# Kernel optimization log

Measured on AMD Instinct MI355X. Metric: run time of the kernel, lower is better.

The kernel has to match this reference:

```python
import jax, jax.numpy as jnp
import numpy as np
import math

B, S, D, H = 2, 2048, 1024, 16
HD = D // H

def setup_inputs() -> dict:
    key = jax.random.key(0)
    ks = jax.random.split(key, 12)
    s = 0.02
    inp = {
        'query': jax.random.normal(ks[0], (B, S, D), jnp.float32),
        'key':   jax.random.normal(ks[1], (B, S, D), jnp.float32),
        'value': jax.random.normal(ks[2], (B, S, D), jnp.float32),
        # causal mask: True = masked out
        'mask': jnp.broadcast_to(~jnp.tril(jnp.ones((S, S), bool)), (B, S, S)),
        'Wq': jax.random.normal(ks[3], (D, D), jnp.float32) * s,
        'bq': jnp.zeros((D,), jnp.float32),
        'Wk': jax.random.normal(ks[4], (D, D), jnp.float32) * s,
        'bk': jnp.zeros((D,), jnp.float32),
        'Wv': jax.random.normal(ks[5], (D, D), jnp.float32) * s,
        'bv': jnp.zeros((D,), jnp.float32),
        'Wo': jax.random.normal(ks[6], (D, D), jnp.float32) * s,
        'bo': jnp.zeros((D,), jnp.float32),
    }
    return inp

def reference(query, key, value, mask, Wq, bq, Wk, bk, Wv, bv, Wo, bo):
    def shape(x):  # [B,S,D] -> [B,H,S,HD]
        return x.reshape(B, -1, H, HD).transpose(0, 2, 1, 3)
    Q = shape(query @ Wq.T + bq) / math.sqrt(HD)
    K = shape(key @ Wk.T + bk)
    V = shape(value @ Wv.T + bv)
    scores = jnp.einsum('bhqd,bhkd->bhqk', Q, K).astype(jnp.float32)
    scores = jnp.where(mask[:, None, :, :], -1e18, scores)
    attn = jax.nn.softmax(scores, axis=-1).astype(query.dtype)
    # dropout p=0 (inference)
    ctx = jnp.einsum('bhqk,bhkd->bhqd', attn, V)
    ctx = ctx.transpose(0, 2, 1, 3).reshape(B, -1, D)
    output = ctx @ Wo.T + bo
    return output, attn
```

## Files before the change

kernel.cpp:

```cpp
#include <hip/hip_runtime.h>
#include <hip/hip_fp16.h>

typedef _Float16 f16;
typedef f16 f16x8 __attribute__((ext_vector_type(8)));
typedef float f32x4 __attribute__((ext_vector_type(4)));

#define MFMA16(a, b, c) __builtin_amdgcn_mfma_f32_16x16x32_f16(a, b, c, 0, 0, 0)

static constexpr int Bn = 2, Sn = 2048, Dn = 1024, Hn = 16, HDn = 64;
static constexpr int Mn = Bn * Sn;

__device__ inline void gload_lds16(const void* g, void* l) {
    __builtin_amdgcn_global_load_lds((const __attribute__((address_space(1))) void*)g,
                                     (__attribute__((address_space(3))) void*)l,
                                     16, 0, 0);
}

__global__ __launch_bounds__(256) void convert_all(
    const float* __restrict__ q, const float* __restrict__ k, const float* __restrict__ v,
    const float* __restrict__ wq, const float* __restrict__ wk, const float* __restrict__ wv,
    const float* __restrict__ wo,
    f16* qo, f16* ko, f16* vo, f16* wqo, f16* wko, f16* wvo, f16* woo) {
    const int c = blockIdx.x * 256 + threadIdx.x;
    const float* src;
    f16* dst;
    int off;
    if (c < 3 * 524288) {
        const int t = c >> 19;
        off = c & 524287;
        src = (t == 0) ? q : (t == 1) ? k : v;
        dst = (t == 0) ? qo : (t == 1) ? ko : vo;
    } else {
        const int c2 = c - 3 * 524288;
        const int t = c2 >> 17;
        off = c2 & 131071;
        src = (t == 0) ? wq : (t == 1) ? wk : (t == 2) ? wv : wo;
        dst = (t == 0) ? wqo : (t == 1) ? wko : (t == 2) ? wvo : woo;
    }
    const float4 a = ((const float4*)src)[off * 2];
    const float4 b = ((const float4*)src)[off * 2 + 1];
    f16x8 r = {(f16)a.x, (f16)a.y, (f16)a.z, (f16)a.w,
               (f16)b.x, (f16)b.y, (f16)b.z, (f16)b.w};
    *(f16x8*)(dst + (size_t)off * 8) = r;
}

struct GemmArgs {
    const f16* X[3];
    const f16* W[3];
    const float* bias[3];
    void* out[3];
    float scale[3];
};

template <bool OUT_F16>
__global__ __launch_bounds__(256) void gemm128(GemmArgs args) {
    __shared__ __align__(16) f16 sbuf[2 * 128 * 64];
    f16* As = sbuf;
    f16* Bs = sbuf + 128 * 64;

    const int z = blockIdx.z;
    const f16* __restrict__ X = args.X[z];
    const f16* __restrict__ W = args.W[z];
    const float* __restrict__ bias = args.bias[z];
    const float scale = args.scale[z];

    const int tid = threadIdx.x, w = tid >> 6, lane = tid & 63;
    const int lr = lane & 15, lg = lane >> 4;
    const int m0 = blockIdx.y * 128, n0 = blockIdx.x * 128;
    const int wm = (w >> 1) * 64, wn = (w & 1) * 64;

    const int srow = w * 32 + (lane >> 3);
    const int scol = (lane & 7) * 8;

    f32x4 acc[4][4] = {};

    for (int k0 = 0; k0 < Dn; k0 += 64) {
        __syncthreads();
#pragma unroll
        for (int j = 0; j < 4; ++j) {
            gload_lds16(X + (size_t)(m0 + srow + j * 8) * Dn + k0 + scol,
                        &As[(w * 4 + j) * 512]);
            gload_lds16(W + (size_t)(n0 + srow + j * 8) * Dn + k0 + scol,
                        &Bs[(w * 4 + j) * 512]);
        }
        __syncthreads();

#pragma unroll
        for (int half = 0; half < 2; ++half) {
            f16x8 a[4], b[4];
#pragma unroll
            for (int mi = 0; mi < 4; ++mi)
                a[mi] = *(const f16x8*)&As[(wm + mi * 16 + lr) * 64 + half * 32 + lg * 8];
#pragma unroll
            for (int ni = 0; ni < 4; ++ni)
                b[ni] = *(const f16x8*)&Bs[(wn + ni * 16 + lr) * 64 + half * 32 + lg * 8];
#pragma unroll
            for (int mi = 0; mi < 4; ++mi)
#pragma unroll
                for (int ni = 0; ni < 4; ++ni)
                    acc[mi][ni] = MFMA16(a[mi], b[ni], acc[mi][ni]);
        }
    }

    float bv[4];
#pragma unroll
    for (int ni = 0; ni < 4; ++ni) bv[ni] = bias[n0 + wn + ni * 16 + lr];

    if (OUT_F16) {
        __syncthreads();
#pragma unroll
        for (int mi = 0; mi < 4; ++mi)
#pragma unroll
            for (int ni = 0; ni < 4; ++ni)
#pragma unroll
                for (int j = 0; j < 4; ++j)
                    sbuf[(wm + mi * 16 + lg * 4 + j) * 128 + wn + ni * 16 + lr] =
                        (f16)((acc[mi][ni][j] + bv[ni]) * scale);
        __syncthreads();
        f16* out = (f16*)args.out[z];
#pragma unroll
        for (int t = 0; t < 8; ++t) {
            const int idx = t * 256 + tid;
            const int r = idx >> 4, cc = (idx & 15) * 8;
            *(f16x8*)(out + (size_t)(m0 + r) * Dn + n0 + cc) = *(f16x8*)&sbuf[r * 128 + cc];
        }
    } else {
        float* out = (float*)args.out[z];
#pragma unroll
        for (int mi = 0; mi < 4; ++mi)
#pragma unroll
            for (int ni = 0; ni < 4; ++ni)
#pragma unroll
                for (int j = 0; j < 4; ++j)
                    out[(size_t)(m0 + wm + mi * 16 + lg * 4 + j) * Dn + n0 + wn + ni * 16 + lr] =
                        (acc[mi][ni][j] + bv[ni]) * scale;
    }
}

__global__ __launch_bounds__(256) void flash_ctx(const f16* __restrict__ Qh,
                                                 const f16* __restrict__ Kh,
                                                 const f16* __restrict__ Vh,
                                                 f16* __restrict__ ctx,
                                                 float* __restrict__ rinv_g) {
    __shared__ __align__(16) f16 Qs[64][72];
    __shared__ __align__(16) f16 Ks[64][72];
    __shared__ __align__(16) f16 Vs[64][72];
    __shared__ __align__(16) f16 Ps[4][16][72];

    const int tid = threadIdx.x, w = tid >> 6, lane = tid & 63;
    const int lr = lane & 15, lg = lane >> 4;
    const int qt = blockIdx.x;
    const int bh = blockIdx.y;
    const int b = bh >> 4, h = bh & 15;

    const f16* Qb = Qh + (size_t)b * Sn * Dn + h * HDn;
    const f16* Kb = Kh + (size_t)b * Sn * Dn + h * HDn;
    const f16* Vb = Vh + (size_t)b * Sn * Dn + h * HDn;

    for (int i = tid; i < 512; i += 256) {
        const int r = i >> 3, dq = i & 7;
        *(f16x8*)&Qs[r][dq * 8] = *(const f16x8*)(Qb + (size_t)(qt * 64 + r) * Dn + dq * 8);
    }
    __syncthreads();
    f16x8 qa0 = *(const f16x8*)&Qs[w * 16 + lr][lg * 8];
    f16x8 qa1 = *(const f16x8*)&Qs[w * 16 + lr][lg * 8 + 32];

    float lsum[4] = {0.f, 0.f, 0.f, 0.f};
    f32x4 octx[4] = {};

    for (int kt = 0; kt <= qt; ++kt) {
        __syncthreads();
        for (int i = tid; i < 512; i += 256) {
            const int r = i >> 3, dq = i & 7;
            *(f16x8*)&Ks[r][dq * 8] = *(const f16x8*)(Kb + (size_t)(kt * 64 + r) * Dn + dq * 8);
        }
        for (int i = tid; i < 512; i += 256) {
            const int kk = i & 63, dq = i >> 6;
            f16x8 v = *(const f16x8*)(Vb + (size_t)(kt * 64 + kk) * Dn + dq * 8);
#pragma unroll
            for (int j = 0; j < 8; ++j) Vs[dq * 8 + j][kk] = v[j];
        }
        __syncthreads();

        const bool diag = (kt == qt);
#pragma unroll
        for (int nf = 0; nf < 4; ++nf) {
            f16x8 kb0 = *(const f16x8*)&Ks[nf * 16 + lr][lg * 8];
            f16x8 kb1 = *(const f16x8*)&Ks[nf * 16 + lr][lg * 8 + 32];
            f32x4 a = {};
            a = MFMA16(qa0, kb0, a);
            a = MFMA16(qa1, kb1, a);
#pragma unroll
            for (int j = 0; j < 4; ++j) {
                const int qr = w * 16 + lg * 4 + j;
                const int kc = nf * 16 + lr;
                const bool masked = diag && (kc > qr);
                const float p = masked ? 0.f : __expf(a[j]);
                lsum[j] += p;
                Ps[w][lg * 4 + j][kc] = (f16)p;
            }
        }

        f16x8 pa0 = *(const f16x8*)&Ps[w][lr][lg * 8];
        f16x8 pa1 = *(const f16x8*)&Ps[w][lr][lg * 8 + 32];
#pragma unroll
        for (int df = 0; df < 4; ++df) {
            f16x8 vb0 = *(const f16x8*)&Vs[df * 16 + lr][lg * 8];
            f16x8 vb1 = *(const f16x8*)&Vs[df * 16 + lr][lg * 8 + 32];
            octx[df] = MFMA16(pa0, vb0, octx[df]);
            octx[df] = MFMA16(pa1, vb1, octx[df]);
        }
    }

    float rv[4];
#pragma unroll
    for (int j = 0; j < 4; ++j) {
        float s = lsum[j];
        s += __shfl_xor(s, 1);
        s += __shfl_xor(s, 2);
        s += __shfl_xor(s, 4);
        s += __shfl_xor(s, 8);
        rv[j] = 1.0f / s;
    }

#pragma unroll
    for (int df = 0; df < 4; ++df) {
#pragma unroll
        for (int j = 0; j < 4; ++j) {
            const int sq = qt * 64 + w * 16 + lg * 4 + j;
            const int d = df * 16 + lr;
            ctx[((size_t)b * Sn + sq) * Dn + h * HDn + d] = (f16)(octx[df][j] * rv[j]);
        }
    }
    if (lr == 0) {
#pragma unroll
        for (int j = 0; j < 4; ++j)
            rinv_g[(size_t)bh * Sn + qt * 64 + w * 16 + lg * 4 + j] = rv[j];
    }
}

__global__ __launch_bounds__(256) void attn_write(const f16* __restrict__ Qh,
                                                  const f16* __restrict__ Kh,
                                                  const float* __restrict__ rinv_g,
                                                  float* __restrict__ attn) {
    __shared__ __align__(16) f16 Qs[64][72];
    __shared__ __align__(16) f16 Ks[64][72];
    __shared__ __align__(16) float Pf[64][68];

    const int tid = threadIdx.x, w = tid >> 6, lane = tid & 63;
    const int lr = lane & 15, lg = lane >> 4;
    const int qt = blockIdx.x;
    const int bh = blockIdx.y;
    const int b = bh >> 4, h = bh & 15;

    const f16* Qb = Qh + (size_t)b * Sn * Dn + h * HDn;
    const f16* Kb = Kh + (size_t)b * Sn * Dn + h * HDn;
    float* attn_base = attn + ((size_t)bh * Sn + qt * 64) * Sn;

    for (int i = tid; i < 512; i += 256) {
        const int r = i >> 3, dq = i & 7;
        *(f16x8*)&Qs[r][dq * 8] = *(const f16x8*)(Qb + (size_t)(qt * 64 + r) * Dn + dq * 8);
    }

    float rv[4];
#pragma unroll
    for (int j = 0; j < 4; ++j)
        rv[j] = rinv_g[(size_t)bh * Sn + qt * 64 + w * 16 + lg * 4 + j];

    __syncthreads();
    f16x8 qa0 = *(const f16x8*)&Qs[w * 16 + lr][lg * 8];
    f16x8 qa1 = *(const f16x8*)&Qs[w * 16 + lr][lg * 8 + 32];

    for (int kt = 0; kt <= qt; ++kt) {
        __syncthreads();
        for (int i = tid; i < 512; i += 256) {
            const int r = i >> 3, dq = i & 7;
            *(f16x8*)&Ks[r][dq * 8] = *(const f16x8*)(Kb + (size_t)(kt * 64 + r) * Dn + dq * 8);
        }
        __syncthreads();

        const bool diag = (kt == qt);
#pragma unroll
        for (int nf = 0; nf < 4; ++nf) {
            f16x8 kb0 = *(const f16x8*)&Ks[nf * 16 + lr][lg * 8];
            f16x8 kb1 = *(const f16x8*)&Ks[nf * 16 + lr][lg * 8 + 32];
            f32x4 a = {};
            a = MFMA16(qa0, kb0, a);
            a = MFMA16(qa1, kb1, a);
#pragma unroll
            for (int j = 0; j < 4; ++j) {
                const int qr = w * 16 + lg * 4 + j;
                const int kc = nf * 16 + lr;
                const bool masked = diag && (kc > qr);
                Pf[qr][kc] = masked ? 0.f : __expf(a[j]) * rv[j];
            }
        }
        __syncthreads();

#pragma unroll
        for (int t = 0; t < 4; ++t) {
            const int idx = t * 256 + tid;
            const int r = idx >> 4, c = (idx & 15) * 4;
            *(float4*)(attn_base + (size_t)r * Sn + kt * 64 + c) = *(float4*)&Pf[r][c];
        }
    }

    const int colstart = (qt + 1) * 64;
    const int width4 = (Sn - colstart) >> 2;
    const float4 z = {0.f, 0.f, 0.f, 0.f};
    for (int r = 0; r < 64; ++r) {
        float4* dst = (float4*)(attn_base + (size_t)r * Sn + colstart);
        for (int c = tid; c < width4; c += 256) dst[c] = z;
    }
}

extern "C" void kernel_launch(void* const* d_in, const int* in_sizes, int n_in,
                              void* d_out, int out_size, void* d_ws, size_t ws_size,
                              hipStream_t stream) {
    const float* query = (const float*)d_in[0];
    const float* key   = (const float*)d_in[1];
    const float* value = (const float*)d_in[2];
    const float* Wq = (const float*)d_in[4];
    const float* bq = (const float*)d_in[5];
    const float* Wk = (const float*)d_in[6];
    const float* bk = (const float*)d_in[7];
    const float* Wv = (const float*)d_in[8];
    const float* bv = (const float*)d_in[9];
    const float* Wo = (const float*)d_in[10];
    const float* bo = (const float*)d_in[11];

    const size_t mk = (size_t)Mn * Dn;
    const size_t nk = (size_t)Dn * Dn;
    f16* p = (f16*)d_ws;
    f16 *Xq16 = p, *Xk16 = p + mk, *Xv16 = p + 2 * mk;
    f16 *Wq16 = p + 3 * mk, *Wk16 = Wq16 + nk, *Wv16 = Wq16 + 2 * nk, *Wo16 = Wq16 + 3 * nk;
    f16 *Qh = Wq16 + 4 * nk, *Kh = Qh + mk, *Vh = Qh + 2 * mk, *ctx = Qh + 3 * mk;
    float* rinv_g = (float*)(ctx + mk);

    float* out_f  = (float*)d_out;
    float* attn_f = out_f + (size_t)Bn * Sn * Dn;

    hipLaunchKernelGGL(convert_all, dim3(8192), dim3(256), 0, stream,
                       query, key, value, Wq, Wk, Wv, Wo,
                       Xq16, Xk16, Xv16, Wq16, Wk16, Wv16, Wo16);

    GemmArgs qkv;
    qkv.X[0] = Xq16; qkv.X[1] = Xk16; qkv.X[2] = Xv16;
    qkv.W[0] = Wq16; qkv.W[1] = Wk16; qkv.W[2] = Wv16;
    qkv.bias[0] = bq; qkv.bias[1] = bk; qkv.bias[2] = bv;
    qkv.out[0] = Qh; qkv.out[1] = Kh; qkv.out[2] = Vh;
    qkv.scale[0] = 0.125f; qkv.scale[1] = 1.0f; qkv.scale[2] = 1.0f;
    hipLaunchKernelGGL((gemm128<true>), dim3(Dn / 128, Mn / 128, 3), dim3(256), 0, stream, qkv);

    hipLaunchKernelGGL(flash_ctx, dim3(Sn / 64, Bn * Hn), dim3(256), 0, stream,
                       Qh, Kh, Vh, ctx, rinv_g);

    GemmArgs oproj;
    oproj.X[0] = ctx; oproj.X[1] = ctx; oproj.X[2] = ctx;
    oproj.W[0] = Wo16; oproj.W[1] = Wo16; oproj.W[2] = Wo16;
    oproj.bias[0] = bo; oproj.bias[1] = bo; oproj.bias[2] = bo;
    oproj.out[0] = out_f; oproj.out[1] = out_f; oproj.out[2] = out_f;
    oproj.scale[0] = 1.0f; oproj.scale[1] = 1.0f; oproj.scale[2] = 1.0f;
    hipLaunchKernelGGL((gemm128<false>), dim3(Dn / 128, Mn / 128, 1), dim3(256), 0, stream, oproj);

    hipLaunchKernelGGL(attn_write, dim3(Sn / 64, Bn * Hn), dim3(256), 0, stream,
                       Qh, Kh, rinv_g, attn_f);
}
```

Baseline: 339.1 us.

## Swizzle LDS tiles, pre-transpose V, widen flash tiles, fuse out-proj with attn write

Adds XOR-swizzled LDS layouts so global_load_lds can stage GEMM and attention tiles without bank conflicts. The QKV GEMM now writes V already transposed per head, removing the scalar transpose inside the flash kernel. The flash kernel uses 512 threads over 128 query rows and schedules the largest tiles first. The output projection and the attention-probability write are merged into one launch, and probabilities are stored straight to global memory instead of being staged in LDS. The cost is larger code and uncoalesced scalar stores for the attention matrix.

```diff
diff --git a/kernel.cpp b/kernel.cpp
--- a/kernel.cpp
+++ b/kernel.cpp
@@ -14,6 +14,10 @@
     __builtin_amdgcn_global_load_lds((const __attribute__((address_space(1))) void*)g,
                                      (__attribute__((address_space(3))) void*)l,
                                      16, 0, 0);
+}
+
+__device__ inline int swz(int row, int chunk) {
+    return row * 64 + ((chunk ^ (row & 7)) * 8);
 }
 
 __global__ __launch_bounds__(256) void convert_all(
@@ -50,27 +54,28 @@
     const float* bias[3];
     void* out[3];
     float scale[3];
+    int mode[3];
 };
 
-template <bool OUT_F16>
-__global__ __launch_bounds__(256) void gemm128(GemmArgs args) {
-    __shared__ __align__(16) f16 sbuf[2 * 128 * 64];
+__global__ __launch_bounds__(256) void gemm_qkv(GemmArgs args) {
+    __shared__ __align__(16) f16 sbuf[17408];
     f16* As = sbuf;
-    f16* Bs = sbuf + 128 * 64;
+    f16* Bs = sbuf + 8192;
 
     const int z = blockIdx.z;
     const f16* __restrict__ X = args.X[z];
     const f16* __restrict__ W = args.W[z];
     const float* __restrict__ bias = args.bias[z];
     const float scale = args.scale[z];
+    const int mode = args.mode[z];
 
     const int tid = threadIdx.x, w = tid >> 6, lane = tid & 63;
     const int lr = lane & 15, lg = lane >> 4;
     const int m0 = blockIdx.y * 128, n0 = blockIdx.x * 128;
     const int wm = (w >> 1) * 64, wn = (w & 1) * 64;
 
-    const int srow = w * 32 + (lane >> 3);
-    const int scol = (lane & 7) * 8;
+    const int dr = lane >> 3;
+    const int schunk = (lane & 7) ^ dr;
 
     f32x4 acc[4][4] = {};
 
@@ -78,9 +83,9 @@
         __syncthreads();
 #pragma unroll
         for (int j = 0; j < 4; ++j) {
-            gload_lds16(X + (size_t)(m0 + srow + j * 8) * Dn + k0 + scol,
+            gload_lds16(X + (size_t)(m0 + w * 32 + j * 8 + dr) * Dn + k0 + schunk * 8,
                         &As[(w * 4 + j) * 512]);
-            gload_lds16(W + (size_t)(n0 + srow + j * 8) * Dn + k0 + scol,
+            gload_lds16(W + (size_t)(n0 + w * 32 + j * 8 + dr) * Dn + k0 + schunk * 8,
                         &Bs[(w * 4 + j) * 512]);
         }
         __syncthreads();
@@ -90,10 +95,10 @@
             f16x8 a[4], b[4];
 #pragma unroll
             for (int mi = 0; mi < 4; ++mi)
-                a[mi] = *(const f16x8*)&As[(wm + mi * 16 + lr) * 64 + half * 32 + lg * 8];
+                a[mi] = *(const f16x8*)&As[swz(wm + mi * 16 + lr, half * 4 + lg)];
 #pragma unroll
             for (int ni = 0; ni < 4; ++ni)
-                b[ni] = *(const f16x8*)&Bs[(wn + ni * 16 + lr) * 64 + half * 32 + lg * 8];
+                b[ni] = *(const f16x8*)&Bs[swz(wn + ni * 16 + lr, half * 4 + lg)];
 #pragma unroll
             for (int mi = 0; mi < 4; ++mi)
 #pragma unroll
@@ -106,15 +111,15 @@
 #pragma unroll
     for (int ni = 0; ni < 4; ++ni) bv[ni] = bias[n0 + wn + ni * 16 + lr];
 
-    if (OUT_F16) {
-        __syncthreads();
+    __syncthreads();
+    if (mode == 0) {
 #pragma unroll
         for (int mi = 0; mi < 4; ++mi)
 #pragma unroll
             for (int ni = 0; ni < 4; ++ni)
 #pragma unroll
                 for (int j = 0; j < 4; ++j)
-                    sbuf[(wm + mi * 16 + lg * 4 + j) * 128 + wn + ni * 16 + lr] =
+                    sbuf[(wm + mi * 16 + lg * 4 + j) * 136 + wn + ni * 16 + lr] =
                         (f16)((acc[mi][ni][j] + bv[ni]) * scale);
         __syncthreads();
         f16* out = (f16*)args.out[z];
@@ -122,93 +127,96 @@
         for (int t = 0; t < 8; ++t) {
             const int idx = t * 256 + tid;
             const int r = idx >> 4, cc = (idx & 15) * 8;
-            *(f16x8*)(out + (size_t)(m0 + r) * Dn + n0 + cc) = *(f16x8*)&sbuf[r * 128 + cc];
+            *(f16x8*)(out + (size_t)(m0 + r) * Dn + n0 + cc) = *(f16x8*)&sbuf[r * 136 + cc];
         }
     } else {
-        float* out = (float*)args.out[z];
 #pragma unroll
         for (int mi = 0; mi < 4; ++mi)
 #pragma unroll
             for (int ni = 0; ni < 4; ++ni)
 #pragma unroll
                 for (int j = 0; j < 4; ++j)
-                    out[(size_t)(m0 + wm + mi * 16 + lg * 4 + j) * Dn + n0 + wn + ni * 16 + lr] =
-                        (acc[mi][ni][j] + bv[ni]) * scale;
-    }
-}
-
-__global__ __launch_bounds__(256) void flash_ctx(const f16* __restrict__ Qh,
+                    sbuf[(wn + ni * 16 + lr) * 136 + wm + mi * 16 + lg * 4 + j] =
+                        (f16)((acc[mi][ni][j] + bv[ni]) * scale);
+        __syncthreads();
+        f16* out = (f16*)args.out[z];
+        const int b = m0 >> 11, s0 = m0 & (Sn - 1);
+#pragma unroll
+        for (int t = 0; t < 8; ++t) {
+            const int idx = t * 256 + tid;
+            const int nn = idx >> 4, cc = (idx & 15) * 8;
+            const int n = n0 + nn;
+            const int hh = n >> 6, d = n & 63;
+            *(f16x8*)(out + (((size_t)(b * Hn + hh) * HDn + d) * Sn) + s0 + cc) =
+                *(f16x8*)&sbuf[nn * 136 + cc];
+        }
+    }
+}
+
+__global__ __launch_bounds__(512) void flash_ctx(const f16* __restrict__ Qh,
                                                  const f16* __restrict__ Kh,
-                                                 const f16* __restrict__ Vh,
+                                                 const f16* __restrict__ Vt,
                                                  f16* __restrict__ ctx,
                                                  float* __restrict__ rinv_g) {
-    __shared__ __align__(16) f16 Qs[64][72];
-    __shared__ __align__(16) f16 Ks[64][72];
-    __shared__ __align__(16) f16 Vs[64][72];
-    __shared__ __align__(16) f16 Ps[4][16][72];
+    __shared__ __align__(16) f16 Qs[8192];
+    __shared__ __align__(16) f16 Ks[4096];
+    __shared__ __align__(16) f16 Vts[4096];
+    __shared__ __align__(16) f16 Ps[8 * 16 * 72];
 
     const int tid = threadIdx.x, w = tid >> 6, lane = tid & 63;
     const int lr = lane & 15, lg = lane >> 4;
-    const int qt = blockIdx.x;
+    const int qt = (Sn / 128 - 1) - blockIdx.x;
     const int bh = blockIdx.y;
     const int b = bh >> 4, h = bh & 15;
 
+    const int dr = lane >> 3;
+    const int schunk = (lane & 7) ^ dr;
+
     const f16* Qb = Qh + (size_t)b * Sn * Dn + h * HDn;
     const f16* Kb = Kh + (size_t)b * Sn * Dn + h * HDn;
-    const f16* Vb = Vh + (size_t)b * Sn * Dn + h * HDn;
-
-    for (int i = tid; i < 512; i += 256) {
-        const int r = i >> 3, dq = i & 7;
-        *(f16x8*)&Qs[r][dq * 8] = *(const f16x8*)(Qb + (size_t)(qt * 64 + r) * Dn + dq * 8);
-    }
+    const f16* Vtb = Vt + (size_t)bh * HDn * Sn;
+
+#pragma unroll
+    for (int i = 0; i < 2; ++i)
+        gload_lds16(Qb + (size_t)(qt * 128 + w * 16 + i * 8 + dr) * Dn + schunk * 8,
+                    &Qs[(w * 16 + i * 8) * 64]);
     __syncthreads();
-    f16x8 qa0 = *(const f16x8*)&Qs[w * 16 + lr][lg * 8];
-    f16x8 qa1 = *(const f16x8*)&Qs[w * 16 + lr][lg * 8 + 32];
+    f16x8 qa[2];
+#pragma unroll
+    for (int kh = 0; kh < 2; ++kh)
+        qa[kh] = *(const f16x8*)&Qs[swz(w * 16 + lr, kh * 4 + lg)];
 
     float lsum[4] = {0.f, 0.f, 0.f, 0.f};
     f32x4 octx[4] = {};
-
-    for (int kt = 0; kt <= qt; ++kt) {
-        __syncthreads();
-        for (int i = tid; i < 512; i += 256) {
-            const int r = i >> 3, dq = i & 7;
-            *(f16x8*)&Ks[r][dq * 8] = *(const f16x8*)(Kb + (size_t)(kt * 64 + r) * Dn + dq * 8);
-        }
-        for (int i = tid; i < 512; i += 256) {
-            const int kk = i & 63, dq = i >> 6;
-            f16x8 v = *(const f16x8*)(Vb + (size_t)(kt * 64 + kk) * Dn + dq * 8);
-#pragma unroll
-            for (int j = 0; j < 8; ++j) Vs[dq * 8 + j][kk] = v[j];
-        }
-        __syncthreads();
-
-        const bool diag = (kt == qt);
+    const int ktmax = 2 * qt + 1;
+
+    for (int kt = 0; kt <= ktmax; ++kt) {
+        __syncthreads();
+        gload_lds16(Kb + (size_t)(kt * 64 + w * 8 + dr) * Dn + schunk * 8, &Ks[w * 512]);
+        gload_lds16(Vtb + (size_t)(w * 8 + dr) * Sn + kt * 64 + schunk * 8, &Vts[w * 512]);
+        __syncthreads();
+
 #pragma unroll
         for (int nf = 0; nf < 4; ++nf) {
-            f16x8 kb0 = *(const f16x8*)&Ks[nf * 16 + lr][lg * 8];
-            f16x8 kb1 = *(const f16x8*)&Ks[nf * 16 + lr][lg * 8 + 32];
             f32x4 a = {};
-            a = MFMA16(qa0, kb0, a);
-            a = MFMA16(qa1, kb1, a);
+            a = MFMA16(qa[0], *(const f16x8*)&Ks[swz(nf * 16 + lr, lg)], a);
+            a = MFMA16(qa[1], *(const f16x8*)&Ks[swz(nf * 16 + lr, 4 + lg)], a);
 #pragma unroll
             for (int j = 0; j < 4; ++j) {
-                const int qr = w * 16 + lg * 4 + j;
-                const int kc = nf * 16 + lr;
-                const bool masked = diag && (kc > qr);
-                const float p = masked ? 0.f : __expf(a[j]);
+                const int qg = qt * 128 + w * 16 + lg * 4 + j;
+                const int kg = kt * 64 + nf * 16 + lr;
+                const float p = (kg > qg) ? 0.f : __expf(a[j]);
                 lsum[j] += p;
-                Ps[w][lg * 4 + j][kc] = (f16)p;
+                Ps[w * 1152 + (lg * 4 + j) * 72 + nf * 16 + lr] = (f16)p;
             }
         }
 
-        f16x8 pa0 = *(const f16x8*)&Ps[w][lr][lg * 8];
-        f16x8 pa1 = *(const f16x8*)&Ps[w][lr][lg * 8 + 32];
+        f16x8 pa0 = *(const f16x8*)&Ps[w * 1152 + lr * 72 + lg * 8];
+        f16x8 pa1 = *(const f16x8*)&Ps[w * 1152 + lr * 72 + 32 + lg * 8];
 #pragma unroll
         for (int df = 0; df < 4; ++df) {
-            f16x8 vb0 = *(const f16x8*)&Vs[df * 16 + lr][lg * 8];
-            f16x8 vb1 = *(const f16x8*)&Vs[df * 16 + lr][lg * 8 + 32];
-            octx[df] = MFMA16(pa0, vb0, octx[df]);
-            octx[df] = MFMA16(pa1, vb1, octx[df]);
+            octx[df] = MFMA16(pa0, *(const f16x8*)&Vts[swz(df * 16 + lr, lg)], octx[df]);
+            octx[df] = MFMA16(pa1, *(const f16x8*)&Vts[swz(df * 16 + lr, 4 + lg)], octx[df]);
         }
     }
 
@@ -224,43 +232,98 @@
     }
 
 #pragma unroll
-    for (int df = 0; df < 4; ++df) {
+    for (int df = 0; df < 4; ++df)
 #pragma unroll
         for (int j = 0; j < 4; ++j) {
-            const int sq = qt * 64 + w * 16 + lg * 4 + j;
-            const int d = df * 16 + lr;
-            ctx[((size_t)b * Sn + sq) * Dn + h * HDn + d] = (f16)(octx[df][j] * rv[j]);
-        }
-    }
+            const int sq = qt * 128 + w * 16 + lg * 4 + j;
+            ctx[((size_t)b * Sn + sq) * Dn + h * HDn + df * 16 + lr] =
+                (f16)(octx[df][j] * rv[j]);
+        }
     if (lr == 0) {
 #pragma unroll
         for (int j = 0; j < 4; ++j)
-            rinv_g[(size_t)bh * Sn + qt * 64 + w * 16 + lg * 4 + j] = rv[j];
-    }
-}
-
-__global__ __launch_bounds__(256) void attn_write(const f16* __restrict__ Qh,
+            rinv_g[(size_t)bh * Sn + qt * 128 + w * 16 + lg * 4 + j] = rv[j];
+    }
+}
+
+__global__ __launch_bounds__(256) void tail_fused(const f16* __restrict__ Qh,
                                                   const f16* __restrict__ Kh,
                                                   const float* __restrict__ rinv_g,
-                                                  float* __restrict__ attn) {
-    __shared__ __align__(16) f16 Qs[64][72];
-    __shared__ __align__(16) f16 Ks[64][72];
-    __shared__ __align__(16) float Pf[64][68];
+                                                  float* __restrict__ attn,
+                                                  const f16* __restrict__ ctxX,
+                                                  const f16* __restrict__ Wo,
+                                                  const float* __restrict__ bo,
+                                                  float* __restrict__ out_f) {
+    __shared__ __align__(16) f16 lds_[16384];
 
     const int tid = threadIdx.x, w = tid >> 6, lane = tid & 63;
     const int lr = lane & 15, lg = lane >> 4;
-    const int qt = blockIdx.x;
-    const int bh = blockIdx.y;
+    const int dr = lane >> 3;
+    const int schunk = (lane & 7) ^ dr;
+
+    if (blockIdx.x < 256) {
+        f16* As = lds_;
+        f16* Bs = lds_ + 8192;
+        const int n0 = (blockIdx.x & 7) * 128, m0 = (blockIdx.x >> 3) * 128;
+        const int wm = (w >> 1) * 64, wn = (w & 1) * 64;
+
+        f32x4 acc[4][4] = {};
+        for (int k0 = 0; k0 < Dn; k0 += 64) {
+            __syncthreads();
+#pragma unroll
+            for (int j = 0; j < 4; ++j) {
+                gload_lds16(ctxX + (size_t)(m0 + w * 32 + j * 8 + dr) * Dn + k0 + schunk * 8,
+                            &As[(w * 4 + j) * 512]);
+                gload_lds16(Wo + (size_t)(n0 + w * 32 + j * 8 + dr) * Dn + k0 + schunk * 8,
+                            &Bs[(w * 4 + j) * 512]);
+            }
+            __syncthreads();
+#pragma unroll
+            for (int half = 0; half < 2; ++half) {
+                f16x8 a[4], b[4];
+#pragma unroll
+                for (int mi = 0; mi < 4; ++mi)
+                    a[mi] = *(const f16x8*)&As[swz(wm + mi * 16 + lr, half * 4 + lg)];
+#pragma unroll
+                for (int ni = 0; ni < 4; ++ni)
+                    b[ni] = *(const f16x8*)&Bs[swz(wn + ni * 16 + lr, half * 4 + lg)];
+#pragma unroll
+                for (int mi = 0; mi < 4; ++mi)
+#pragma unroll
+                    for (int ni = 0; ni < 4; ++ni)
+                        acc[mi][ni] = MFMA16(a[mi], b[ni], acc[mi][ni]);
+            }
+        }
+        float bv[4];
+#pragma unroll
+        for (int ni = 0; ni < 4; ++ni) bv[ni] = bo[n0 + wn + ni * 16 + lr];
+#pragma unroll
+        for (int mi = 0; mi < 4; ++mi)
+#pragma unroll
+            for (int ni = 0; ni < 4; ++ni)
+#pragma unroll
+                for (int j = 0; j < 4; ++j)
+                    out_f[(size_t)(m0 + wm + mi * 16 + lg * 4 + j) * Dn + n0 + wn + ni * 16 + lr] =
+                        acc[mi][ni][j] + bv[ni];
+        return;
+    }
+
+    const int bid = blockIdx.x - 256;
+    const int qt = 31 - (bid & 31);
+    const int bh = bid >> 5;
     const int b = bh >> 4, h = bh & 15;
+
+    f16* Qs = lds_;
+    f16* Ks = lds_ + 4096;
 
     const f16* Qb = Qh + (size_t)b * Sn * Dn + h * HDn;
     const f16* Kb = Kh + (size_t)b * Sn * Dn + h * HDn;
     float* attn_base = attn + ((size_t)bh * Sn + qt * 64) * Sn;
 
-    for (int i = tid; i < 512; i += 256) {
-        const int r = i >> 3, dq = i & 7;
-        *(f16x8*)&Qs[r][dq * 8] = *(const f16x8*)(Qb + (size_t)(qt * 64 + r) * Dn + dq * 8);
-    }
+#pragma unroll
+    for (int i = 0; i < 2; ++i)
+        gload_lds16(Qb + (size_t)(qt * 64 + w * 16 + i * 8 + dr) * Dn + schunk * 8,
+                    &Qs[(w * 16 + i * 8) * 64]);
 
     float rv[4];
 #pragma unroll
@@ -268,40 +331,32 @@
         rv[j] = rinv_g[(size_t)bh * Sn + qt * 64 + w * 16 + lg * 4 + j];
 
     __syncthreads();
-    f16x8 qa0 = *(const f16x8*)&Qs[w * 16 + lr][lg * 8];
-    f16x8 qa1 = *(const f16x8*)&Qs[w * 16 + lr][lg * 8 + 32];
+    f16x8 qa[2];
+#pragma unroll
+    for (int kh = 0; kh < 2; ++kh)
+        qa[kh] = *(const f16x8*)&Qs[swz(w * 16 + lr, kh * 4 + lg)];
 
     for (int kt = 0; kt <= qt; ++kt) {
         __syncthreads();
-        for (int i = tid; i < 512; i += 256) {
-            const int r = i >> 3, dq = i & 7;
-            *(f16x8*)&Ks[r][dq * 8] = *(const f16x8*)(Kb + (size_t)(kt * 64 + r) * Dn + dq * 8);
-        }
+#pragma unroll
+        for (int i = 0; i < 2; ++i)
+            gload_lds16(Kb + (size_t)(kt * 64 + w * 16 + i * 8 + dr) * Dn + schunk * 8,
+                        &Ks[(w * 16 + i * 8) * 64]);
         __syncthreads();
 
         const bool diag = (kt == qt);
 #pragma unroll
         for (int nf = 0; nf < 4; ++nf) {
-            f16x8 kb0 = *(const f16x8*)&Ks[nf * 16 + lr][lg * 8];
-            f16x8 kb1 = *(const f16x8*)&Ks[nf * 16 + lr][lg * 8 + 32];
             f32x4 a = {};
-            a = MFMA16(qa0, kb0, a);
-            a = MFMA16(qa1, kb1, a);
+            a = MFMA16(qa[0], *(const f16x8*)&Ks[swz(nf * 16 + lr, lg)], a);
+            a = MFMA16(qa[1], *(const f16x8*)&Ks[swz(nf * 16 + lr, 4 + lg)], a);
 #pragma unroll
             for (int j = 0; j < 4; ++j) {
                 const int qr = w * 16 + lg * 4 + j;
                 const int kc = nf * 16 + lr;
-                const bool masked = diag && (kc > qr);
-                Pf[qr][kc] = masked ? 0.f : __expf(a[j]) * rv[j];
+                const float p = (diag && kc > qr) ? 0.f : __expf(a[j]) * rv[j];
+                attn_base[(size_t)qr * Sn + kt * 64 + kc] = p;
             }
-        }
-        __syncthreads();
-
-#pragma unroll
-        for (int t = 0; t < 4; ++t) {
-            const int idx = t * 256 + tid;
-            const int r = idx >> 4, c = (idx & 15) * 4;
-            *(float4*)(attn_base + (size_t)r * Sn + kt * 64 + c) = *(float4*)&Pf[r][c];
         }
     }
 
@@ -334,7 +389,7 @@
     f16* p = (f16*)d_ws;
     f16 *Xq16 = p, *Xk16 = p + mk, *Xv16 = p + 2 * mk;
     f16 *Wq16 = p + 3 * mk, *Wk16 = Wq16 + nk, *Wv16 = Wq16 + 2 * nk, *Wo16 = Wq16 + 3 * nk;
-    f16 *Qh = Wq16 + 4 * nk, *Kh = Qh + mk, *Vh = Qh + 2 * mk, *ctx = Qh + 3 * mk;
+    f16 *Qh = Wq16 + 4 * nk, *Kh = Qh + mk, *Vt = Qh + 2 * mk, *ctx = Qh + 3 * mk;
     float* rinv_g = (float*)(ctx + mk);
 
     float* out_f  = (float*)d_out;
@@ -348,21 +403,14 @@
     qkv.X[0] = Xq16; qkv.X[1] = Xk16; qkv.X[2] = Xv16;
     qkv.W[0] = Wq16; qkv.W[1] = Wk16; qkv.W[2] = Wv16;
     qkv.bias[0] = bq; qkv.bias[1] = bk; qkv.bias[2] = bv;
-    qkv.out[0] = Qh; qkv.out[1] = Kh; qkv.out[2] = Vh;
+    qkv.out[0] = Qh; qkv.out[1] = Kh; qkv.out[2] = Vt;
     qkv.scale[0] = 0.125f; qkv.scale[1] = 1.0f; qkv.scale[2] = 1.0f;
-    hipLaunchKernelGGL((gemm128<true>), dim3(Dn / 128, Mn / 128, 3), dim3(256), 0, stream, qkv);
-
-    hipLaunchKernelGGL(flash_ctx, dim3(Sn / 64, Bn * Hn), dim3(256), 0, stream,
-                       Qh, Kh, Vh, ctx, rinv_g);
-
-    GemmArgs oproj;
-    oproj.X[0] = ctx; oproj.X[1] = ctx; oproj.X[2] = ctx;
-    oproj.W[0] = Wo16; oproj.W[1] = Wo16; oproj.W[2] = Wo16;
-    oproj.bias[0] = bo; oproj.bias[1] = bo; oproj.bias[2] = bo;
-    oproj.out[0] = out_f; oproj.out[1] = out_f; oproj.out[2] = out_f;
-    oproj.scale[0] = 1.0f; oproj.scale[1] = 1.0f; oproj.scale[2] = 1.0f;
-    hipLaunchKernelGGL((gemm128<false>), dim3(Dn / 128, Mn / 128, 1), dim3(256), 0, stream, oproj);
-
-    hipLaunchKernelGGL(attn_write, dim3(Sn / 64, Bn * Hn), dim3(256), 0, stream,
-                       Qh, Kh, rinv_g, attn_f);
-}
+    qkv.mode[0] = 0; qkv.mode[1] = 0; qkv.mode[2] = 1;
+    hipLaunchKernelGGL(gemm_qkv, dim3(Dn / 128, Mn / 128, 3), dim3(256), 0, stream, qkv);
+
+    hipLaunchKernelGGL(flash_ctx, dim3(Sn / 128, Bn * Hn), dim3(512), 0, stream,
+                       Qh, Kh, Vt, ctx, rinv_g);
+
+    hipLaunchKernelGGL(tail_fused, dim3(256 + 1024), dim3(256), 0, stream,
+                       Qh, Kh, rinv_g, attn_f, ctx, Wo16, bo, out_f);
+}
```

After: 288.9 us. 1.17x faster.
